# Performance work log

Measured on AMD Instinct MI355X. Metric: run time of the kernel, lower is better.

## Reference

```python
import jax, jax.numpy as jnp
import numpy as np
from jax import lax

EPS = 1e-10
NUM_ITERATIONS = 3  # init arg num_iterations
M, R = 16384, 32


def setup_inputs() -> dict:
    key = jax.random.key(0)
    x = jax.random.normal(key, (M, R, 2), dtype=jnp.float32)
    return {"x": x}


def reference(x):
    # x: (M, R, 2) -> complex (M, R); work with QT (R, M) so rows = columns
    r = x.shape[1]
    xc = (x[..., 0] + 1j * x[..., 1]).T  # (R, M) complex64
    idx = jnp.arange(r)

    # --- classical Gram-Schmidt pass (sequential over columns j) ---
    def gs_col(QT, j):
        def proj(v, i):
            qi = QT[i]
            coeff = jnp.sum(jnp.conj(qi) * v) * (i < j)  # only previous cols
            return v - coeff * qi, None
        v, _ = lax.scan(proj, xc[j], idx)
        v = v / jnp.sqrt(jnp.sum(jnp.abs(v) ** 2) + EPS)
        return QT.at[j].set(v), None

    QT, _ = lax.scan(gs_col, jnp.zeros_like(xc), idx)

    # --- iterative refinement sweeps: each column uses the OLD Q -> vmap over j ---
    def refine_col(QT, j):
        def proj(v, i):
            qi = QT[i]
            coeff = jnp.sum(jnp.conj(qi) * v) * (i != j)
            return v - 0.5 * coeff * qi, None
        v, _ = lax.scan(proj, QT[j], idx)
        return v / jnp.sqrt(jnp.sum(jnp.abs(v) ** 2) + EPS)

    for _ in range(NUM_ITERATIONS):
        QT = jax.vmap(refine_col, in_axes=(None, 0))(QT, idx)

    Q = QT.T  # (M, R)
    return jnp.stack([Q.real, Q.imag], axis=-1)
```

## Files before the change

kernel.cpp:

```cpp
#include <hip/hip_runtime.h>


#define M_ROWS 16384

__global__ __launch_bounds__(256) void gram_partial(const float* __restrict__ x,
                                                    float* __restrict__ G8) {
  __shared__ float lds[64 * 64];
  const int t = threadIdx.x;
  const int j = t & 31, g = t >> 5;
  const size_t row0 = (size_t)blockIdx.x * 64;
  float ar[4] = {0.f, 0.f, 0.f, 0.f};
  float ai[4] = {0.f, 0.f, 0.f, 0.f};
  const float4* src = (const float4*)(x + row0 * 64);
  float4* dst = (float4*)lds;
#pragma unroll
  for (int q = 0; q < 4; ++q) dst[t + 256 * q] = src[t + 256 * q];
  __syncthreads();
#pragma unroll 4
  for (int m = 0; m < 64; ++m) {
    const float2* row = (const float2*)(lds + m * 64);
    const float2 xj = row[j];
#pragma unroll
    for (int q = 0; q < 4; ++q) {
      const float2 xi = row[g + q * 8];
      ar[q] += xi.x * xj.x + xi.y * xj.y;
      ai[q] += xi.x * xj.y - xi.y * xj.x;
    }
  }
  float* P = G8 + (size_t)(blockIdx.x & 7) * 2048;
#pragma unroll
  for (int q = 0; q < 4; ++q) {
    const int i = g + q * 8;
    atomicAdd(&P[(i * 32 + j) * 2 + 0], ar[q]);
    atomicAdd(&P[(i * 32 + j) * 2 + 1], ai[q]);
  }
}

__global__ __launch_bounds__(256) void fused_solve(const float* __restrict__ x,
                                                   const float* __restrict__ G8,
                                                   float* __restrict__ out) {
  __shared__ float2 A[1024];
  const int t = threadIdx.x;

#pragma unroll
  for (int e = t; e < 1024; e += 256) {
    float2 s = {0.f, 0.f};
#pragma unroll
    for (int c = 0; c < 8; ++c) {
      const float2 g = ((const float2*)G8)[c * 1024 + e];
      s.x += g.x;
      s.y += g.y;
    }
    A[e] = s;
  }
  __syncthreads();

  for (int k = 0; k < 31; ++k) {
    const float invd = 1.0f / A[k * 32 + k].x;
#pragma unroll
    for (int q = 0; q < 4; ++q) {
      const int e = t + q * 256;
      const int i = e >> 5, j = e & 31;
      if (i > k && j > k && j <= i) {
        const float2 a = A[i * 32 + k];
        const float2 b = A[j * 32 + k];
        float2 v = A[e];
        v.x -= (a.x * b.x + a.y * b.y) * invd;
        v.y -= (a.y * b.x - a.x * b.y) * invd;
        A[e] = v;
      }
    }
    __syncthreads();
  }

  const size_t m = (size_t)blockIdx.x * 256 + t;
  float2 xr[32];
  const float4* xp = (const float4*)(x + m * 64);
#pragma unroll
  for (int q = 0; q < 16; ++q) {
    const float4 v = xp[q];
    xr[2 * q].x = v.x; xr[2 * q].y = v.y;
    xr[2 * q + 1].x = v.z; xr[2 * q + 1].y = v.w;
  }
#pragma unroll
  for (int j = 0; j < 32; ++j) {
    const float d = A[j * 32 + j].x;
    const float invd = 1.0f / d;
    const float invs = 1.0f / sqrtf(d);
    const float2 u = {xr[j].x * invd, xr[j].y * invd};
    xr[j].x *= invs;
    xr[j].y *= invs;
#pragma unroll
    for (int i = j + 1; i < 32; ++i) {
      const float2 l = A[i * 32 + j];
      xr[i].x -= u.x * l.x + u.y * l.y;
      xr[i].y -= u.y * l.x - u.x * l.y;
    }
  }
  float4* op = (float4*)(out + m * 64);
#pragma unroll
  for (int q = 0; q < 16; ++q) {
    float4 v;
    v.x = xr[2 * q].x; v.y = xr[2 * q].y;
    v.z = xr[2 * q + 1].x; v.w = xr[2 * q + 1].y;
    op[q] = v;
  }
}

extern "C" void kernel_launch(void* const* d_in, const int* in_sizes, int n_in,
                              void* d_out, int out_size, void* d_ws, size_t ws_size,
                              hipStream_t stream) {
  const float* x = (const float*)d_in[0];
  float* out = (float*)d_out;
  float* G8 = (float*)d_ws;

  gram_partial<<<256, 256, 0, stream>>>(x, G8);
  fused_solve<<<64, 256, 0, stream>>>(x, G8, out);
}
```

Before: 91.11 us.

## Compute explicit inverse Cholesky factor per block and apply as small matmul

Rewrites the second kernel so each block factorizes the Gram matrix with a single wave and explicitly builds the inverse triangular factor W. It then applies Q = X·W as an LDS-staged complex matmul instead of running a per-row forward substitution. The grid grows from 64 to 256 blocks, and the x tile is loaded into LDS while the factorization runs. The intent is to remove the long serial per-thread triangular solve, which used 32 complex registers per row, and to raise occupancy. In exchange, every block redundantly repeats the factorization and inversion on only 64 threads.

```diff
diff --git a/kernel.cpp b/kernel.cpp
--- a/kernel.cpp
+++ b/kernel.cpp
@@ -36,12 +36,18 @@
   }
 }
 
-__global__ __launch_bounds__(256) void fused_solve(const float* __restrict__ x,
-                                                   const float* __restrict__ G8,
-                                                   float* __restrict__ out) {
-  __shared__ float2 A[1024];
+__global__ __launch_bounds__(256) void fused_winv_apply(
+    const float* __restrict__ x, const float* __restrict__ G8,
+    float* __restrict__ out) {
+  __shared__ float2 A[33 * 32];
+  __shared__ float wlds[2048];
+  __shared__ float xs[4096];
   const int t = threadIdx.x;
 
+  const float4* xp = (const float4*)(x + (size_t)blockIdx.x * 4096);
+  float4* xd = (float4*)xs;
+#pragma unroll
+  for (int q = 0; q < 4; ++q) xd[t + 256 * q] = xp[t + 256 * q];
 #pragma unroll
   for (int e = t; e < 1024; e += 256) {
     float2 s = {0.f, 0.f};
@@ -51,59 +57,74 @@
       s.x += g.x;
       s.y += g.y;
     }
-    A[e] = s;
+    A[(e & 31) * 33 + (e >> 5)] = s;
   }
   __syncthreads();
 
-  for (int k = 0; k < 31; ++k) {
-    const float invd = 1.0f / A[k * 32 + k].x;
+  if (t < 64) {
+    const int j = t & 31, ig = t >> 5;
+    for (int k = 0; k < 31; ++k) {
+      const float invd = 1.0f / A[k * 33 + k].x;
+      const float2 ajk = A[k * 33 + j];
+      const float2 cjk = {ajk.x * invd, -ajk.y * invd};
+      for (int q = (k + 1) >> 1; q < 16; ++q) {
+        const int i = ig + 2 * q;
+        if (i > k && j > k && j <= i) {
+          const float2 aik = A[k * 33 + i];
+          float2 v = A[j * 33 + i];
+          v.x -= aik.x * cjk.x - aik.y * cjk.y;
+          v.y -= aik.x * cjk.y + aik.y * cjk.x;
+          A[j * 33 + i] = v;
+        }
+      }
+      __builtin_amdgcn_wave_barrier();
+    }
+    const int c = j;
+    float2 w[32];
 #pragma unroll
-    for (int q = 0; q < 4; ++q) {
-      const int e = t + q * 256;
-      const int i = e >> 5, j = e & 31;
-      if (i > k && j > k && j <= i) {
-        const float2 a = A[i * 32 + k];
-        const float2 b = A[j * 32 + k];
-        float2 v = A[e];
-        v.x -= (a.x * b.x + a.y * b.y) * invd;
-        v.y -= (a.y * b.x - a.x * b.y) * invd;
-        A[e] = v;
+    for (int i = 0; i < 32; ++i) w[i] = {0.f, 0.f};
+    w[c].x = 1.0f / sqrtf(A[c * 33 + c].x);
+#pragma unroll
+    for (int i = 30; i >= 0; --i) {
+      float2 s = {0.f, 0.f};
+#pragma unroll
+      for (int k = i + 1; k < 32; ++k) {
+        const float2 a = A[i * 33 + k];
+        s.x += a.x * w[k].x + a.y * w[k].y;
+        s.y += a.x * w[k].y - a.y * w[k].x;
+      }
+      const float invd = 1.0f / A[i * 33 + i].x;
+      if (i != c) {
+        w[i].x = -s.x * invd;
+        w[i].y = -s.y * invd;
       }
     }
-    __syncthreads();
-  }
-
-  const size_t m = (size_t)blockIdx.x * 256 + t;
-  float2 xr[32];
-  const float4* xp = (const float4*)(x + m * 64);
+    if (t < 32) {
 #pragma unroll
-  for (int q = 0; q < 16; ++q) {
-    const float4 v = xp[q];
-    xr[2 * q].x = v.x; xr[2 * q].y = v.y;
-    xr[2 * q + 1].x = v.z; xr[2 * q + 1].y = v.w;
-  }
-#pragma unroll
-  for (int j = 0; j < 32; ++j) {
-    const float d = A[j * 32 + j].x;
-    const float invd = 1.0f / d;
-    const float invs = 1.0f / sqrtf(d);
-    const float2 u = {xr[j].x * invd, xr[j].y * invd};
-    xr[j].x *= invs;
-    xr[j].y *= invs;
-#pragma unroll
-    for (int i = j + 1; i < 32; ++i) {
-      const float2 l = A[i * 32 + j];
-      xr[i].x -= u.x * l.x + u.y * l.y;
-      xr[i].y -= u.y * l.x - u.x * l.y;
+      for (int i = 0; i < 32; ++i)
+        ((float2*)wlds)[i * 32 + c] = w[i];
     }
   }
-  float4* op = (float4*)(out + m * 64);
+  __syncthreads();
+
+  const int mg = t >> 4, jp = t & 15;
 #pragma unroll
-  for (int q = 0; q < 16; ++q) {
-    float4 v;
-    v.x = xr[2 * q].x; v.y = xr[2 * q].y;
-    v.z = xr[2 * q + 1].x; v.w = xr[2 * q + 1].y;
-    op[q] = v;
+  for (int g = 0; g < 4; ++g) {
+    const int mloc = mg + g * 16;
+    const float2* xrow = (const float2*)(xs + mloc * 64);
+    float2 a0 = {0.f, 0.f}, a1 = {0.f, 0.f};
+#pragma unroll
+    for (int i = 0; i < 32; ++i) {
+      const float2 xi = xrow[i];
+      const float4 wv = ((const float4*)(wlds + i * 64))[jp];
+      a0.x += xi.x * wv.x - xi.y * wv.y;
+      a0.y += xi.x * wv.y + xi.y * wv.x;
+      a1.x += xi.x * wv.z - xi.y * wv.w;
+      a1.y += xi.x * wv.w + xi.y * wv.z;
+    }
+    float4 o;
+    o.x = a0.x; o.y = a0.y; o.z = a1.x; o.w = a1.y;
+    ((float4*)out)[(size_t)blockIdx.x * 1024 + g * 256 + t] = o;
   }
 }
 
@@ -115,5 +136,5 @@
   float* G8 = (float*)d_ws;
 
   gram_partial<<<256, 256, 0, stream>>>(x, G8);
-  fused_solve<<<64, 256, 0, stream>>>(x, G8, out);
+  fused_winv_apply<<<256, 256, 0, stream>>>(x, G8, out);
 }
```

Result: slower. 117.6 us (+29.1%).

## Split solve into 256 small blocks with wave-level shuffle Cholesky and LDS-staged I/O

Applied to the files above, without the earlier changes.

Replaces the 64-block, 256-thread solve kernel with 256 blocks of 64 threads. Each block factors the Gram matrix inside a single wavefront, one column per lane, using register arrays and shuffles instead of 31 block-wide barrier steps. Input rows are staged through padded shared memory so global loads and stores are coalesced rather than strided per-thread float4 accesses. In exchange, every block redundantly repeats the Cholesky factorization, and each block runs only one wave.

```diff
diff --git a/kernel.cpp b/kernel.cpp
--- a/kernel.cpp
+++ b/kernel.cpp
@@ -36,55 +36,70 @@
   }
 }
 
-__global__ __launch_bounds__(256) void fused_solve(const float* __restrict__ x,
-                                                   const float* __restrict__ G8,
-                                                   float* __restrict__ out) {
-  __shared__ float2 A[1024];
+__global__ __launch_bounds__(64) void chol_solve(const float* __restrict__ x,
+                                                 const float* __restrict__ G8,
+                                                 float* __restrict__ out) {
+  __shared__ float4 Gl[512];
+  __shared__ float2 Acm[34 * 32];
+  __shared__ float4 xsp[64 * 17];
   const int t = threadIdx.x;
 
+  const float4* xp = (const float4*)(x + (size_t)blockIdx.x * 4096);
 #pragma unroll
-  for (int e = t; e < 1024; e += 256) {
-    float2 s = {0.f, 0.f};
+  for (int s = 0; s < 16; ++s) {
+    const int g = t + 64 * s;
+    xsp[(g >> 4) * 17 + (g & 15)] = xp[g];
+  }
+  const float4* G8f4 = (const float4*)G8;
 #pragma unroll
-    for (int c = 0; c < 8; ++c) {
-      const float2 g = ((const float2*)G8)[c * 1024 + e];
-      s.x += g.x;
-      s.y += g.y;
+  for (int s = 0; s < 8; ++s) {
+    const int g = t + 64 * s;
+    float4 acc = G8f4[g];
+#pragma unroll
+    for (int c = 1; c < 8; ++c) {
+      const float4 p = G8f4[c * 512 + g];
+      acc.x += p.x; acc.y += p.y; acc.z += p.z; acc.w += p.w;
     }
-    A[e] = s;
+    Gl[g] = acc;
   }
   __syncthreads();
 
-  for (int k = 0; k < 31; ++k) {
-    const float invd = 1.0f / A[k * 32 + k].x;
+  if (t < 32) {
+    const int j = t;
+    float2 a[32];
 #pragma unroll
-    for (int q = 0; q < 4; ++q) {
-      const int e = t + q * 256;
-      const int i = e >> 5, j = e & 31;
-      if (i > k && j > k && j <= i) {
-        const float2 a = A[i * 32 + k];
-        const float2 b = A[j * 32 + k];
-        float2 v = A[e];
-        v.x -= (a.x * b.x + a.y * b.y) * invd;
-        v.y -= (a.y * b.x - a.x * b.y) * invd;
-        A[e] = v;
+    for (int i = 0; i < 32; ++i) a[i] = ((const float2*)Gl)[i * 32 + j];
+#pragma unroll
+    for (int k = 0; k < 31; ++k) {
+      const float invd = 1.0f / __shfl(a[k].x, k);
+      const float ux = a[k].x * invd;
+      const float uy = a[k].y * invd;
+      const bool act = (j > k);
+#pragma unroll
+      for (int i = k + 1; i < 32; ++i) {
+        const float cr = __shfl(a[i].x, k);
+        const float ci = __shfl(a[i].y, k);
+        if (act) {
+          a[i].x -= cr * ux - ci * uy;
+          a[i].y -= cr * uy + ci * ux;
+        }
       }
     }
-    __syncthreads();
+#pragma unroll
+    for (int i = 0; i < 32; ++i) Acm[j * 34 + i] = a[i];
   }
+  __syncthreads();
 
-  const size_t m = (size_t)blockIdx.x * 256 + t;
   float2 xr[32];
-  const float4* xp = (const float4*)(x + m * 64);
 #pragma unroll
   for (int q = 0; q < 16; ++q) {
-    const float4 v = xp[q];
+    const float4 v = xsp[t * 17 + q];
     xr[2 * q].x = v.x; xr[2 * q].y = v.y;
     xr[2 * q + 1].x = v.z; xr[2 * q + 1].y = v.w;
   }
 #pragma unroll
   for (int j = 0; j < 32; ++j) {
-    const float d = A[j * 32 + j].x;
+    const float d = Acm[j * 34 + j].x;
     const float invd = 1.0f / d;
     const float invs = 1.0f / sqrtf(d);
     const float2 u = {xr[j].x * invd, xr[j].y * invd};
@@ -92,18 +107,24 @@
     xr[j].y *= invs;
 #pragma unroll
     for (int i = j + 1; i < 32; ++i) {
-      const float2 l = A[i * 32 + j];
+      const float2 l = Acm[j * 34 + i];
       xr[i].x -= u.x * l.x + u.y * l.y;
       xr[i].y -= u.y * l.x - u.x * l.y;
     }
   }
-  float4* op = (float4*)(out + m * 64);
 #pragma unroll
   for (int q = 0; q < 16; ++q) {
     float4 v;
     v.x = xr[2 * q].x; v.y = xr[2 * q].y;
     v.z = xr[2 * q + 1].x; v.w = xr[2 * q + 1].y;
-    op[q] = v;
+    xsp[t * 17 + q] = v;
+  }
+  __syncthreads();
+  float4* op = (float4*)(out + (size_t)blockIdx.x * 4096);
+#pragma unroll
+  for (int s = 0; s < 16; ++s) {
+    const int g = t + 64 * s;
+    op[g] = xsp[(g >> 4) * 17 + (g & 15)];
   }
 }
 
@@ -115,5 +136,5 @@
   float* G8 = (float*)d_ws;
 
   gram_partial<<<256, 256, 0, stream>>>(x, G8);
-  fused_solve<<<64, 256, 0, stream>>>(x, G8, out);
+  chol_solve<<<256, 64, 0, stream>>>(x, G8, out);
 }
```

Result: slower. 101.6 us (+11.5%).
